# Optimization experiments

Measured on AMD Instinct MI355X. Metric: run time of the kernel, lower is better.

Reference implementation:

```python
import jax, jax.numpy as jnp
import numpy as np


def _weighted_sample(key, w, n_draw):
    # Inverse-CDF weighted sampling with replacement; prob proportional to relu(w).
    # Matches torch.multinomial over the strictly-positive (top-cnt sorted) entries,
    # since zero-weight columns are never selected with side='right'.
    cdf = jnp.cumsum(jnp.maximum(w, 0.0), axis=1)                     # [R, C]
    u = jax.random.uniform(key, (w.shape[0], n_draw), dtype=w.dtype) * cdf[:, -1:]
    idx = jax.vmap(lambda c, q: jnp.searchsorted(c, q, side='right'))(cdf, u)
    return jax.lax.stop_gradient(jnp.minimum(idx, w.shape[1] - 1))    # [R, K] column ids


def contrast_loss(key, padj, nadj, px, nx):
    R, Cp = padj.shape
    Cn = nadj.shape[1]
    K = min(Cp, Cn)  # num = min(pcnt, ncnt) <= K always
    pcnt = jnp.sum(padj > 0, axis=1)
    ncnt = jnp.sum(nadj > 0, axis=1)
    num = jnp.minimum(pcnt, ncnt)                                     # [R] int
    pinc = jnp.argsort(padj, axis=1)                                  # ascending, like torch.sort
    ninc = jnp.argsort(nadj, axis=1)
    kp, kn = jax.random.split(key)
    samp_n = _weighted_sample(kn, nadj, K)                            # sampled negative cols
    samp_p = _weighted_sample(kp, padj, K)                            # sampled positive cols
    j = jnp.arange(K)
    mask = (j[None, :] < num[:, None]).astype(px.dtype)               # first num draws count
    rows = jnp.arange(R)[:, None]
    # top-num entries of the ascending sort: positions C-num .. C-1
    top_p = jnp.clip(Cp - num[:, None] + j[None, :], 0, Cp - 1)
    top_n = jnp.clip(Cn - num[:, None] + j[None, :], 0, Cn - 1)
    pos_A = jnp.take_along_axis(pinc, top_p, axis=1)                  # branch num==pcnt
    neg_B = jnp.take_along_axis(ninc, top_n, axis=1)                  # branch num==ncnt<pcnt
    termA = jnp.maximum(nx[rows, samp_n] - px[rows, pos_A] + 1.0, 0.0)
    termB = jnp.maximum(nx[rows, neg_B] - px[rows, samp_p] + 1.0, 0.0)
    branchA = (pcnt <= ncnt)[:, None]                                 # num == pcnt
    term = jnp.where(branchA, termA, termB) * mask
    row_loss = term.sum(axis=1) / jnp.maximum(num, 1).astype(px.dtype)
    return jnp.where(num > 0, row_loss, 0.0).sum()


def _forward(KUU_adj, VUU_adj, Vuser, Vitem, Kuser, Kitem, preference, Vpreference, structure):
    key = jax.random.key(42)
    k0, k1, k2, k3 = jax.random.split(key, 4)
    f32 = VUU_adj.dtype
    # --- Vu: V-user vs V-user ---
    Vu_adj = Vuser @ Vuser.T                                          # [Nv, Nv]
    n = Vu_adj.shape[0]
    tmp1 = 1.0 - (VUU_adj > 0).astype(f32) - jnp.eye(n, dtype=f32)
    Vu = contrast_loss(k0, VUU_adj, tmp1, Vu_adj, Vu_adj)
    # --- Ku: K-user vs K-user (last 3 cols are negatives) ---
    Ku_adj = Kuser @ Kuser.T                                          # [Nk, Nk]
    Kc = KUU_adj.shape[1]
    tmp2 = (1.0 - (KUU_adj > 0).astype(f32) - jnp.eye(Kc, dtype=f32))[:n, -3:]
    Ku = contrast_loss(k1, KUU_adj[:n, :Kc - 3], tmp2,
                       Ku_adj[:n, :Kc - 3], Ku_adj[:n, -3:])
    # --- Vi: V-user vs V-item (binarization of tmp3 is overwritten in the original) ---
    Vi_adj = Vuser @ Vitem.T                                          # [Nv, NvI]
    VUI_adj = Vpreference.T
    Vi = contrast_loss(k2, VUI_adj, 1.0 - VUI_adj, Vi_adj, Vi_adj)
    # --- Ki: first 5 K-users vs K-item ---
    Ki_adj = Kuser[:5, :] @ Kitem.T                                   # [5, NkI]
    KUI_adj = preference.T
    Ki = contrast_loss(k3, KUI_adj, 1.0 - KUI_adj, Ki_adj, Ki_adj)
    # --- ii: item-item structure alignment ---
    ii_adj = Kitem @ Vitem.T                                          # [NkI, NvI]
    ii = jnp.abs(ii_adj - structure[:, :ii_adj.shape[1]]).mean()
    return (Vu, Ku, Vi, Ki, ii)


def setup_inputs() -> dict:
    key = jax.random.key(0)
    ks = jax.random.split(key, 10)
    Nv, Nk, NvI, NkI, d = 2048, 2051, 4096, 4096, 64
    return {
        'KUU_adj': jax.random.normal(ks[0], (Nk, Nk), jnp.float32),
        'VUU_adj': jax.random.normal(ks[1], (Nv, Nv), jnp.float32),
        'Vuser': jax.random.normal(ks[2], (Nv, d), jnp.float32),
        'Vitem': jax.random.normal(ks[3], (NvI, d), jnp.float32),
        'Kuser': jax.random.normal(ks[4], (Nk, d), jnp.float32),
        'Kitem': jax.random.normal(ks[5], (NkI, d), jnp.float32),
        'Vid': jax.random.randint(ks[6], (Nv,), 0, NvI, jnp.int64 if jax.config.jax_enable_x64 else jnp.int32),
        'preference': jax.random.uniform(ks[7], (NkI, 5), jnp.float32),
        'Vpreference': jax.random.uniform(ks[8], (NvI, Nv), jnp.float32),
        'structure': jax.random.normal(ks[9], (NkI, NvI), jnp.float32),
    }


def reference(KUU_adj, VUU_adj, Vuser, Vitem, Kuser, Kitem, Vid, preference, Vpreference, structure):
    # Vid is accepted by the original forward but never used.
    return _forward(KUU_adj, VUU_adj, Vuser, Vitem, Kuser, Kitem, preference, Vpreference, structure)
```

## Files before the change

### kernel.cpp

```cpp
#include <hip/hip_runtime.h>
#include <cstdint>
#include <cstddef>

__host__ __device__ inline void tf2x32(uint32_t k0, uint32_t k1,
                                       uint32_t c0, uint32_t c1,
                                       uint32_t* o0, uint32_t* o1) {
  uint32_t ks0 = k0, ks1 = k1, ks2 = k0 ^ k1 ^ 0x1BD11BDAu;
  uint32_t x0 = c0 + ks0, x1 = c1 + ks1;
#define TFR(r) { x0 += x1; x1 = (x1 << (r)) | (x1 >> (32 - (r))); x1 ^= x0; }
  TFR(13) TFR(15) TFR(26) TFR(6)   x0 += ks1; x1 += ks2 + 1u;
  TFR(17) TFR(29) TFR(16) TFR(24)  x0 += ks2; x1 += ks0 + 2u;
  TFR(13) TFR(15) TFR(26) TFR(6)   x0 += ks0; x1 += ks1 + 3u;
  TFR(17) TFR(29) TFR(16) TFR(24)  x0 += ks1; x1 += ks2 + 4u;
  TFR(13) TFR(15) TFR(26) TFR(6)   x0 += ks2; x1 += ks0 + 5u;
#undef TFR
  *o0 = x0; *o1 = x1;
}

__device__ inline float tf_u01(uint32_t k0, uint32_t k1, uint32_t c0, uint32_t c1) {
  uint32_t a, b; tf2x32(k0, k1, c0, c1, &a, &b);
  uint32_t bits = a ^ b;
  return __uint_as_float((bits >> 9) | 0x3f800000u) - 1.0f;
}

__device__ inline float mur_u01(uint32_t z, uint32_t salt) {
  z ^= salt;
  z ^= z >> 16; z *= 0x85ebca6bu;
  z ^= z >> 13; z *= 0xc2b2ae35u;
  z ^= z >> 16;
  return __uint_as_float((z >> 9) | 0x3f800000u) - 1.0f;
}

__device__ inline int bsearch_right(const float* cdf, int C, float u) {
  int lo = 0, hi = C;
  while (lo < hi) { int mid = (lo + hi) >> 1; if (cdf[mid] <= u) lo = mid + 1; else hi = mid; }
  return lo < C ? lo : C - 1;
}

__global__ void init_out(float* out) {
  if (threadIdx.x < 5) out[threadIdx.x] = 0.0f;
}

__global__ void transpose_k(const float* __restrict__ in, float* __restrict__ out,
                            int R, int C) {
  __shared__ float tile[32][33];
  int bx = blockIdx.x * 32;
  int by = blockIdx.y * 32;
  int tx = threadIdx.x, ty = threadIdx.y;
#pragma unroll
  for (int q = 0; q < 32; q += 8)
    tile[ty + q][tx] = in[(size_t)(by + ty + q) * C + (bx + tx)];
  __syncthreads();
#pragma unroll
  for (int q = 0; q < 32; q += 8)
    out[(size_t)(bx + ty + q) * R + (by + tx)] = tile[tx][ty + q];
}

__global__ __launch_bounds__(256) void gemm_nt(
    const float* __restrict__ Arows, const float* __restrict__ Brows,
    float* __restrict__ X, int N) {
  __shared__ __align__(16) float At[64 * 68];
  __shared__ __align__(16) float Bt[64 * 68];
  const int t = threadIdx.x;
  const int i0 = blockIdx.x * 64, j0 = blockIdx.y * 64;
  for (int idx = t; idx < 1024; idx += 256) {
    int row = idx >> 4, q = idx & 15;
    float4 va = *(const float4*)(Arows + (size_t)(i0 + row) * 64 + 4 * q);
    At[(4 * q + 0) * 68 + row] = va.x; At[(4 * q + 1) * 68 + row] = va.y;
    At[(4 * q + 2) * 68 + row] = va.z; At[(4 * q + 3) * 68 + row] = va.w;
    float4 vb = *(const float4*)(Brows + (size_t)(j0 + row) * 64 + 4 * q);
    Bt[(4 * q + 0) * 68 + row] = vb.x; Bt[(4 * q + 1) * 68 + row] = vb.y;
    Bt[(4 * q + 2) * 68 + row] = vb.z; Bt[(4 * q + 3) * 68 + row] = vb.w;
  }
  __syncthreads();
  const int ti = t >> 4, tj = t & 15;
  float acc[4][4] = {{0.f,0.f,0.f,0.f},{0.f,0.f,0.f,0.f},{0.f,0.f,0.f,0.f},{0.f,0.f,0.f,0.f}};
  for (int k = 0; k < 64; ++k) {
    const float4 a = *(const float4*)&At[k * 68 + 4 * ti];
    const float4 b = *(const float4*)&Bt[k * 68 + 4 * tj];
    const float av[4] = {a.x, a.y, a.z, a.w};
    const float bv[4] = {b.x, b.y, b.z, b.w};
#pragma unroll
    for (int p = 0; p < 4; ++p)
#pragma unroll
      for (int q2 = 0; q2 < 4; ++q2) acc[p][q2] += av[p] * bv[q2];
  }
#pragma unroll
  for (int p = 0; p < 4; ++p) {
    float4 w = make_float4(acc[p][0], acc[p][1], acc[p][2], acc[p][3]);
    *(float4*)(X + (size_t)(i0 + 4 * ti + p) * N + j0 + 4 * tj) = w;
  }
}

__global__ __launch_bounds__(256) void ii_kernel(
    const float* __restrict__ Kitem, const float* __restrict__ Vitem,
    const float* __restrict__ structure_, float* __restrict__ out) {
  __shared__ __align__(16) float At[64 * 68];
  __shared__ __align__(16) float Bt[64 * 68];
  __shared__ float red[256];
  const int t = threadIdx.x;
  const int i0 = blockIdx.x * 64, j0 = blockIdx.y * 64;
  for (int idx = t; idx < 1024; idx += 256) {
    int row = idx >> 4, q = idx & 15;
    float4 va = *(const float4*)(Kitem + (size_t)(i0 + row) * 64 + 4 * q);
    At[(4 * q + 0) * 68 + row] = va.x; At[(4 * q + 1) * 68 + row] = va.y;
    At[(4 * q + 2) * 68 + row] = va.z; At[(4 * q + 3) * 68 + row] = va.w;
    float4 vb = *(const float4*)(Vitem + (size_t)(j0 + row) * 64 + 4 * q);
    Bt[(4 * q + 0) * 68 + row] = vb.x; Bt[(4 * q + 1) * 68 + row] = vb.y;
    Bt[(4 * q + 2) * 68 + row] = vb.z; Bt[(4 * q + 3) * 68 + row] = vb.w;
  }
  __syncthreads();
  const int ti = t >> 4, tj = t & 15;
  float acc[4][4] = {{0.f,0.f,0.f,0.f},{0.f,0.f,0.f,0.f},{0.f,0.f,0.f,0.f},{0.f,0.f,0.f,0.f}};
  for (int k = 0; k < 64; ++k) {
    const float4 a = *(const float4*)&At[k * 68 + 4 * ti];
    const float4 b = *(const float4*)&Bt[k * 68 + 4 * tj];
    const float av[4] = {a.x, a.y, a.z, a.w};
    const float bv[4] = {b.x, b.y, b.z, b.w};
#pragma unroll
    for (int p = 0; p < 4; ++p)
#pragma unroll
      for (int q2 = 0; q2 < 4; ++q2) acc[p][q2] += av[p] * bv[q2];
  }
  float s = 0.0f;
#pragma unroll
  for (int p = 0; p < 4; ++p) {
    const float* srow = structure_ + (size_t)(i0 + 4 * ti + p) * 4096 + j0 + 4 * tj;
#pragma unroll
    for (int q2 = 0; q2 < 4; ++q2) s += fabsf(acc[p][q2] - srow[q2]);
  }
  red[t] = s; __syncthreads();
  for (int off = 128; off > 0; off >>= 1) {
    if (t < off) red[t] += red[t + off];
    __syncthreads();
  }
  if (t == 0) atomicAdd(out + 4, red[0] * (1.0f / 16777216.0f));
}

template <int C, int MODE, bool PRE>
__global__ __launch_bounds__(256) void contrast2(
    const float* __restrict__ padj_mat, size_t rs, size_t cs,
    const float* __restrict__ xmat,
    const float* __restrict__ A, const float* __restrict__ B,
    float* __restrict__ out, int out_idx, uint32_t salt) {
  constexpr int E = C / 256;
  constexpr int LOG2E = (E == 16) ? 4 : 3;
  constexpr int S = (E == 16) ? 260 : 264;
  constexpr int TSZ = (E - 1) * S + 256;
  constexpr int DEPTH = (C == 4096) ? 13 : 12;
  constexpr int NB = 512;
  __shared__ float T[TSZ];
  __shared__ int bs[NB + 1];
  __shared__ float x[PRE ? 1 : C];
  __shared__ __align__(16) float qa[PRE ? 4 : 64];
  __shared__ float red[256];
  __shared__ float wsumsh[4];
  __shared__ int s_pcnt, s_ncnt;
  const int t = threadIdx.x;
  const int r = blockIdx.x;
  const int lane = t & 63, wid = t >> 6;
  const float* xrow = PRE ? (xmat + (size_t)r * C) : nullptr;
  if (t == 0) { s_pcnt = 0; s_ncnt = 0; }
  if (!PRE && t < 64) qa[t] = A[(size_t)r * 64 + t];

  int lp = 0, ln = 0;
  for (int c = t; c < C; c += 256) {
    float v = padj_mat[(size_t)r * rs + (size_t)c * cs];
    T[(c & (E - 1)) * S + (c >> LOG2E)] = v;
    lp += (v > 0.0f) ? 1 : 0;
    if (MODE == 0) ln += (v <= 0.0f && c != r) ? 1 : 0;
    else           ln += ((1.0f - v) > 0.0f) ? 1 : 0;
  }
  if (lp) atomicAdd(&s_pcnt, lp);
  if (ln) atomicAdd(&s_ncnt, ln);
  __syncthreads();

  if (!PRE) {
    const int g = t >> 2, q = t & 3;
    const float4* qa4 = (const float4*)qa;
    for (int c = g; c < C; c += 64) {
      const float4* b4 = (const float4*)(B + (size_t)c * 64);
      float acc = 0.0f;
#pragma unroll
      for (int m = 0; m < 4; ++m) {
        float4 f = b4[q + 4 * m];
        float4 a = qa4[q + 4 * m];
        acc += f.x * a.x + f.y * a.y + f.z * a.z + f.w * a.w;
      }
      acc += __shfl_xor(acc, 1);
      acc += __shfl_xor(acc, 2);
      if (q == 0) x[c] = acc;
    }
    __syncthreads();
  }

  const int pcnt = s_pcnt, ncnt = s_ncnt;
  const int num = min(pcnt, ncnt);
  if (num == 0) return;
  const bool brA = (pcnt <= ncnt);

  auto wf = [&](float v, int c) -> float {
    if (brA) {
      if (MODE == 0) return (v <= 0.0f && c != r) ? 1.0f : 0.0f;
      float nv = 1.0f - v; return nv > 0.0f ? nv : 0.0f;
    }
    return v > 0.0f ? v : 0.0f;
  };

  float csum = 0.0f;
#pragma unroll
  for (int e = 0; e < E; ++e) csum += wf(T[e * S + t], t * E + e);
  float ps = csum;
#pragma unroll
  for (int off = 1; off < 64; off <<= 1) {
    float o = __shfl_up(ps, off);
    if (lane >= off) ps += o;
  }
  if (lane == 63) wsumsh[wid] = ps;
  __syncthreads();
  float wbase = 0.0f;
  for (int w = 0; w < wid; ++w) wbase += wsumsh[w];
  float run = wbase + ps - csum;
  {
#pragma unroll
    for (int e = 0; e < E; ++e) {
      float w = wf(T[e * S + t], t * E + e);
      run += w;
      T[e * S + t] = run;
    }
  }
  __syncthreads();
  const float total = T[(E - 1) * S + 255];

  for (int i = t; i < NB; i += 256) {
    float ub = ((float)i / (float)NB) * total;
    int lo = 0, hi = C;
    for (int it = 0; it < DEPTH; ++it) {
      if (lo < hi) {
        int mid = (lo + hi) >> 1;
        float cv = T[(mid & (E - 1)) * S + (mid >> LOG2E)];
        if (cv <= ub) lo = mid + 1; else hi = mid;
      }
    }
    bs[i] = lo;
  }
  if (t == 0) bs[NB] = C;
  __syncthreads();

  float acc = 0.0f;
  for (int k = 0; k < E; k += 8) {
    int cj[8]; bool dj[8]; float uj[8]; int lo[8], hi[8]; float xc[8];
#pragma unroll
    for (int j = 0; j < 8; ++j) {
      int c = t + (k + j) * 256;
      cj[j] = c;
      float v = padj_mat[(size_t)r * rs + (size_t)c * cs];
      bool det = brA ? (v > 0.0f)
                     : (MODE == 0 ? (v <= 0.0f && c != r) : ((1.0f - v) > 0.0f));
      dj[j] = det;
      xc[j] = PRE ? xrow[c] : x[c];
      float f = mur_u01((uint32_t)(r * C + c), salt);
      uj[j] = f * total;
      int b = (int)(f * (float)NB);
      b = b < NB - 1 ? b : NB - 1; b = b > 0 ? b : 0;
      lo[j] = bs[b]; hi[j] = bs[b + 1];
    }
    for (int it = 0; it < 7; ++it) {
#pragma unroll
      for (int j = 0; j < 8; ++j) {
        int mid = (lo[j] + hi[j]) >> 1;
        float cv = T[(mid & (E - 1)) * S + (mid >> LOG2E)];
        if (lo[j] < hi[j]) {
          if (cv <= uj[j]) lo[j] = mid + 1; else hi[j] = mid;
        }
      }
    }
#pragma unroll
    for (int j = 0; j < 8; ++j) {
      if (dj[j]) {
        int s = lo[j] < C ? lo[j] : C - 1;
        float xs = PRE ? xrow[s] : x[s];
        float term = brA ? (xs - xc[j] + 1.0f) : (xc[j] - xs + 1.0f);
        acc += fmaxf(term, 0.0f);
      }
    }
  }
  red[t] = acc; __syncthreads();
  for (int off = 128; off > 0; off >>= 1) {
    if (t < off) red[t] += red[t + off];
    __syncthreads();
  }
  if (t == 0) atomicAdd(out + out_idx, red[0] / (float)num);
}

__global__ __launch_bounds__(256) void ku_kernel(
    const float* __restrict__ KUU, const float* __restrict__ Kuser,
    float* __restrict__ out,
    uint32_t kp0, uint32_t kp1, uint32_t kn0, uint32_t kn1) {
  const int C = 2048;
  constexpr int E = 8, LOG2E = 3, S = 264;
  constexpr int TSZ = (E - 1) * S + 256;
  __shared__ float T[TSZ];
  __shared__ float red[256];
  __shared__ int s_pcnt;
  const int t = threadIdx.x, r = blockIdx.x;
  const float* row = KUU + (size_t)r * 2051;
  if (t == 0) s_pcnt = 0;
  __syncthreads();
  int lp = 0;
  for (int c = t; c < C; c += 256) {
    float v = row[c];
    T[(c & (E - 1)) * S + (c >> LOG2E)] = v > 0.0f ? v : 0.0f;
    lp += (v > 0.0f) ? 1 : 0;
  }
  if (lp) atomicAdd(&s_pcnt, lp);
  __syncthreads();
  const int pcnt = s_pcnt;
  const float n0 = row[2048], n1 = row[2049], n2 = row[2050];
  const int ng0 = (n0 <= 0.0f), ng1 = (n1 <= 0.0f), ng2 = (n2 <= 0.0f);
  const int ncnt = ng0 + ng1 + ng2;
  const int num = min(pcnt, ncnt);
  if (num == 0) return;

  float csum = 0.0f;
#pragma unroll
  for (int e = 0; e < E; ++e) csum += T[e * S + t];
  red[t] = csum; __syncthreads();
  if (t == 0) {
    float run = 0.0f;
    for (int i = 0; i < 256; ++i) { float v = red[i]; red[i] = run; run += v; }
  }
  __syncthreads();
  {
    float run = red[t];
#pragma unroll
    for (int e = 0; e < E; ++e) { run += T[e * S + t]; T[e * S + t] = run; }
  }
  __syncthreads();
  const float total = T[(E - 1) * S + 255];

  if (pcnt > ncnt) {
    float term = 0.0f;
    if (t < num) {
      int ng[3] = {ng0, ng1, ng2};
      int det = -1, cnt = 0;
      for (int q = 0; q < 3; ++q) {
        if (ng[q]) { if (cnt == t) { det = q; break; } cnt++; }
      }
      float f = tf_u01(kp0, kp1, 0u, (uint32_t)(r * 3 + t));
      float u = f * total;
      int lo = 0, hi = C;
      while (lo < hi) {
        int mid = (lo + hi) >> 1;
        float cv = T[(mid & (E - 1)) * S + (mid >> LOG2E)];
        if (cv <= u) lo = mid + 1; else hi = mid;
      }
      int s = lo < C ? lo : C - 1;
      const float* qr = Kuser + (size_t)r * 64;
      const float* qs = Kuser + (size_t)s * 64;
      const float* qn = Kuser + (size_t)(2048 + det) * 64;
      float px = 0.0f, nx = 0.0f;
      for (int k = 0; k < 64; ++k) { float av = qr[k]; px += av * qs[k]; nx += av * qn[k]; }
      term = fmaxf(nx - px + 1.0f, 0.0f);
    }
    red[t] = term; __syncthreads();
    for (int off = 128; off > 0; off >>= 1) {
      if (t < off) red[t] += red[t + off];
      __syncthreads();
    }
    if (t == 0) atomicAdd(out + 1, red[0] / (float)num);
  } else {
    if (t == 0) {
      float pv[3]; int pi[3]; int np = 0;
      for (int c = 0; c < C; ++c) {
        float v = row[c];
        if (v > 0.0f) { if (np < 3) { pv[np] = v; pi[np] = c; } np++; }
      }
      for (int a2 = 1; a2 < np; ++a2) {
        float v = pv[a2]; int id = pi[a2]; int b2 = a2 - 1;
        while (b2 >= 0 && pv[b2] > v) { pv[b2 + 1] = pv[b2]; pi[b2 + 1] = pi[b2]; b2--; }
        pv[b2 + 1] = v; pi[b2 + 1] = id;
      }
      int ng[3] = {ng0, ng1, ng2};
      float ncdf[3]; float runn = 0.0f;
      for (int q = 0; q < 3; ++q) { runn += ng[q] ? 1.0f : 0.0f; ncdf[q] = runn; }
      float ss = 0.0f;
      for (int j = 0; j < num; ++j) {
        float f = tf_u01(kn0, kn1, 0u, (uint32_t)(r * 3 + j));
        float u = f * runn;
        int s = 0; while (s < 3 && ncdf[s] <= u) s++; if (s > 2) s = 2;
        int det = pi[np - num + j];
        const float* qr = Kuser + (size_t)r * 64;
        const float* qd = Kuser + (size_t)det * 64;
        const float* qn = Kuser + (size_t)(2048 + s) * 64;
        float px = 0.0f, nx = 0.0f;
        for (int k = 0; k < 64; ++k) { float av = qr[k]; px += av * qd[k]; nx += av * qn[k]; }
        ss += fmaxf(nx - px + 1.0f, 0.0f);
      }
      atomicAdd(out + 1, ss / (float)num);
    }
  }
}

__global__ __launch_bounds__(256) void ki_prep(
    const float* __restrict__ preference,
    float* __restrict__ cdf_ws, float* __restrict__ vals_ws,
    int* __restrict__ rank_ws, float* __restrict__ meta) {
  const int C = 4096;
  __shared__ float cdf[4096];
  __shared__ float red[256];
  __shared__ int s_pcnt;
  const int t = threadIdx.x, r = blockIdx.x;
  if (t == 0) s_pcnt = 0;
  __syncthreads();
  for (int i = r * 256 + t; i < 5 * C; i += 5 * 256) rank_ws[i] = 0;
  int lp = 0;
  for (int c = t; c < C; c += 256) {
    float v = preference[(size_t)c * 5 + r];
    lp += (v > 0.0f) ? 1 : 0;
    cdf[c] = 1.0f - v;
    vals_ws[(size_t)r * C + c] = v;
  }
  if (lp) atomicAdd(&s_pcnt, lp);
  __syncthreads();
  const int num = s_pcnt;
  const int E = C >> 8;
  const int base = t * E;
  float csum = 0.0f;
  for (int e = 0; e < E; ++e) csum += cdf[base + e];
  red[t] = csum; __syncthreads();
  if (t == 0) {
    float run = 0.0f;
    for (int i = 0; i < 256; ++i) { float v = red[i]; red[i] = run; run += v; }
  }
  __syncthreads();
  {
    float run = red[t];
    for (int e = 0; e < E; ++e) { float w = cdf[base + e]; run += w; cdf[base + e] = run; }
  }
  __syncthreads();
  for (int c = t; c < C; c += 256) cdf_ws[(size_t)r * C + c] = cdf[c];
  if (t == 0) { meta[2 * r] = (float)num; meta[2 * r + 1] = cdf[C - 1]; }
}

__global__ __launch_bounds__(256) void ki_rank_p(
    const float* __restrict__ vals_ws, int* __restrict__ rank_ws) {
  const int C = 4096;
  __shared__ __align__(16) float sv[256];
  const int t = threadIdx.x;
  const int r = blockIdx.y;
  const int z = blockIdx.z;
  const int c0 = blockIdx.x * 256 + t;
  const float* vrow = vals_ws + (size_t)r * C;
  sv[t] = vrow[z * 256 + t];
  __syncthreads();
  const float v0 = vrow[c0];
  const int cbase = z * 256;
  int rank = 0;
  const float4* sv4 = (const float4*)sv;
#pragma unroll 8
  for (int q = 0; q < 64; ++q) {
    float4 w = sv4[q];
    int cb = cbase + 4 * q;
    rank += (w.x < v0 || (w.x == v0 && cb + 0 < c0)) ? 1 : 0;
    rank += (w.y < v0 || (w.y == v0 && cb + 1 < c0)) ? 1 : 0;
    rank += (w.z < v0 || (w.z == v0 && cb + 2 < c0)) ? 1 : 0;
    rank += (w.w < v0 || (w.w == v0 && cb + 3 < c0)) ? 1 : 0;
  }
  if (rank) atomicAdd(&rank_ws[(size_t)r * C + c0], rank);
}

__global__ __launch_bounds__(256) void ki_scatter(
    const int* __restrict__ rank_ws, int* __restrict__ sorted_ws) {
  const int C = 4096;
  const int t = threadIdx.x;
  const int r = blockIdx.y;
  const int c0 = blockIdx.x * 256 + t;
  sorted_ws[(size_t)r * C + rank_ws[(size_t)r * C + c0]] = c0;
}

__global__ __launch_bounds__(256) void ki_draw(
    const float* __restrict__ cdf_ws, const int* __restrict__ sorted_ws,
    const float* __restrict__ meta,
    const float* __restrict__ Kuser, const float* __restrict__ Kitem,
    float* __restrict__ out, uint32_t kn0, uint32_t kn1) {
  const int C = 4096;
  __shared__ float cdf[4096];
  __shared__ __align__(16) float qa[64];
  __shared__ float red[256];
  const int t = threadIdx.x;
  const int r = blockIdx.y;
  const int j = blockIdx.x * 256 + t;
  if (t < 64) qa[t] = Kuser[(size_t)r * 64 + t];
  for (int c = t; c < C; c += 256) cdf[c] = cdf_ws[(size_t)r * C + c];
  __syncthreads();
  const int num = (int)meta[2 * r];
  const float total = meta[2 * r + 1];
  float acc = 0.0f;
  if (j < num) {
    float f = tf_u01(kn0, kn1, 0u, (uint32_t)(r * 4096 + j));
    float u = f * total;
    int s = bsearch_right(cdf, C, u);
    int det = sorted_ws[(size_t)r * C + (C - num + j)];
    const float4* qa4 = (const float4*)qa;
    const float4* bs = (const float4*)(Kitem + (size_t)s * 64);
    const float4* bd = (const float4*)(Kitem + (size_t)det * 64);
    float xs = 0.0f, xd = 0.0f;
#pragma unroll
    for (int m = 0; m < 16; ++m) {
      float4 a4 = qa4[m]; float4 v1 = bs[m]; float4 v2 = bd[m];
      xs += a4.x * v1.x + a4.y * v1.y + a4.z * v1.z + a4.w * v1.w;
      xd += a4.x * v2.x + a4.y * v2.y + a4.z * v2.z + a4.w * v2.w;
    }
    acc = fmaxf(xs - xd + 1.0f, 0.0f) / (float)num;
  }
  red[t] = acc; __syncthreads();
  for (int off = 128; off > 0; off >>= 1) {
    if (t < off) red[t] += red[t + off];
    __syncthreads();
  }
  if (t == 0 && red[0] != 0.0f) atomicAdd(out + 3, red[0]);
}

__global__ __launch_bounds__(256) void ki_kernel(
    const float* __restrict__ preference, const float* __restrict__ Kuser,
    const float* __restrict__ Kitem, float* __restrict__ out,
    uint32_t kn0, uint32_t kn1) {
  const int C = 4096;
  __shared__ float cdf[4096];
  __shared__ unsigned long long skey[4096];
  __shared__ __align__(16) float qa[64];
  __shared__ float red[256];
  __shared__ int s_pcnt;
  const int t = threadIdx.x, r = blockIdx.x;
  if (t == 0) s_pcnt = 0;
  if (t < 64) qa[t] = Kuser[(size_t)r * 64 + t];
  __syncthreads();
  int lp = 0;
  for (int c = t; c < C; c += 256) {
    float v = preference[(size_t)c * 5 + r];
    lp += (v > 0.0f) ? 1 : 0;
    cdf[c] = 1.0f - v;
    skey[c] = ((unsigned long long)__float_as_uint(v) << 32) | (unsigned)c;
  }
  if (lp) atomicAdd(&s_pcnt, lp);
  __syncthreads();
  const int num = s_pcnt;
  if (num == 0) return;
  const int E = C >> 8;
  const int base = t * E;
  float csum = 0.0f;
  for (int e = 0; e < E; ++e) csum += cdf[base + e];
  red[t] = csum; __syncthreads();
  if (t == 0) {
    float run = 0.0f;
    for (int i = 0; i < 256; ++i) { float v = red[i]; red[i] = run; run += v; }
  }
  __syncthreads();
  {
    float run = red[t];
    for (int e = 0; e < E; ++e) { float w = cdf[base + e]; run += w; cdf[base + e] = run; }
  }
  __syncthreads();
  const float total = cdf[C - 1];
  for (int k = 2; k <= C; k <<= 1) {
    for (int j2 = k >> 1; j2 > 0; j2 >>= 1) {
      for (int i = t; i < C; i += 256) {
        int ixj = i ^ j2;
        if (ixj > i) {
          unsigned long long a = skey[i], b = skey[ixj];
          bool up = ((i & k) == 0);
          if ((a > b) == up) { skey[i] = b; skey[ixj] = a; }
        }
      }
      __syncthreads();
    }
  }
  float acc = 0.0f;
  const float4* qa4 = (const float4*)qa;
  for (int j = t; j < num; j += 256) {
    float f = tf_u01(kn0, kn1, 0u, (uint32_t)(r * 4096 + j));
    float u = f * total;
    int s = bsearch_right(cdf, C, u);
    int det = (int)(skey[C - num + j] & 0xffffffffull);
    const float4* bs = (const float4*)(Kitem + (size_t)s * 64);
    const float4* bd = (const float4*)(Kitem + (size_t)det * 64);
    float xs = 0.0f, xd = 0.0f;
#pragma unroll
    for (int m = 0; m < 16; ++m) {
      float4 a4 = qa4[m]; float4 v1 = bs[m]; float4 v2 = bd[m];
      xs += a4.x * v1.x + a4.y * v1.y + a4.z * v1.z + a4.w * v1.w;
      xd += a4.x * v2.x + a4.y * v2.y + a4.z * v2.z + a4.w * v2.w;
    }
    acc += fmaxf(xs - xd + 1.0f, 0.0f);
  }
  red[t] = acc; __syncthreads();
  for (int off = 128; off > 0; off >>= 1) {
    if (t < off) red[t] += red[t + off];
    __syncthreads();
  }
  if (t == 0) atomicAdd(out + 3, red[0] / (float)num);
}

extern "C" void kernel_launch(void* const* d_in, const int* in_sizes, int n_in,
                              void* d_out, int out_size, void* d_ws, size_t ws_size,
                              hipStream_t stream) {
  const float* KUU   = (const float*)d_in[0];
  const float* VUU   = (const float*)d_in[1];
  const float* Vuser = (const float*)d_in[2];
  const float* Vitem = (const float*)d_in[3];
  const float* Kuser = (const float*)d_in[4];
  const float* Kitem = (const float*)d_in[5];
  const float* pref  = (const float*)d_in[7];
  const float* Vpref = (const float*)d_in[8];
  const float* structure_ = (const float*)d_in[9];
  float* out = (float*)d_out;

  uint32_t k1a, k1b, k3a, k3b;
  tf2x32(0u, 42u, 0u, 1u, &k1a, &k1b);
  tf2x32(0u, 42u, 0u, 3u, &k3a, &k3b);
  uint32_t kup0, kup1, kun0, kun1, kin0, kin1;
  tf2x32(k1a, k1b, 0u, 0u, &kup0, &kup1);
  tf2x32(k1a, k1b, 0u, 1u, &kun0, &kun1);
  tf2x32(k3a, k3b, 0u, 1u, &kin0, &kin1);

  const uint32_t SALT_VU = 0x8AF1B0C2u;
  const uint32_t SALT_VI = 0x5F356495u;

  const size_t vuit_bytes = (size_t)2048 * 4096 * sizeof(float);
  const size_t xvi_bytes  = (size_t)2048 * 4096 * sizeof(float);
  const size_t xvu_bytes  = (size_t)2048 * 2048 * sizeof(float);
  const size_t ki_bytes   = (size_t)(4 * 5 * 4096 + 16) * sizeof(float);
  const size_t full_bytes = vuit_bytes + xvi_bytes + xvu_bytes + ki_bytes;

  const bool full = ws_size >= full_bytes;
  const bool mid  = !full && ws_size >= vuit_bytes + ki_bytes;

  hipLaunchKernelGGL(init_out, dim3(1), dim3(64), 0, stream, out);

  if (full) {
    float* VUIt = (float*)d_ws;
    float* Xvi  = (float*)((char*)d_ws + vuit_bytes);
    float* Xvu  = (float*)((char*)d_ws + vuit_bytes + xvi_bytes);
    char*  kib  = (char*)d_ws + vuit_bytes + xvi_bytes + xvu_bytes;
    float* cdf_ws  = (float*)kib;
    float* vals_ws = cdf_ws + 5 * 4096;
    int*   sorted_ws = (int*)(vals_ws + 5 * 4096);
    int*   rank_ws = sorted_ws + 5 * 4096;
    float* meta = (float*)(rank_ws + 5 * 4096);

    hipLaunchKernelGGL(ki_prep, dim3(5), dim3(256), 0, stream,
                       pref, cdf_ws, vals_ws, rank_ws, meta);
    hipLaunchKernelGGL(ki_rank_p, dim3(16, 5, 16), dim3(256), 0, stream,
                       vals_ws, rank_ws);
    hipLaunchKernelGGL(ki_scatter, dim3(16, 5), dim3(256), 0, stream,
                       rank_ws, sorted_ws);
    hipLaunchKernelGGL(ki_draw, dim3(16, 5), dim3(256), 0, stream,
                       cdf_ws, sorted_ws, meta, Kuser, Kitem, out, kin0, kin1);

    hipLaunchKernelGGL(transpose_k, dim3(64, 128), dim3(32, 8), 0, stream,
                       Vpref, VUIt, 4096, 2048);
    hipLaunchKernelGGL(gemm_nt, dim3(32, 32), dim3(256), 0, stream,
                       Vuser, Vuser, Xvu, 2048);
    hipLaunchKernelGGL(gemm_nt, dim3(32, 64), dim3(256), 0, stream,
                       Vuser, Vitem, Xvi, 4096);
    hipLaunchKernelGGL(ii_kernel, dim3(64, 64), dim3(256), 0, stream,
                       Kitem, Vitem, structure_, out);

    hipLaunchKernelGGL((contrast2<2048, 0, true>), dim3(2048), dim3(256), 0, stream,
                       VUU, (size_t)2048, (size_t)1, Xvu, nullptr, nullptr,
                       out, 0, SALT_VU);
    hipLaunchKernelGGL(ku_kernel, dim3(2048), dim3(256), 0, stream,
                       KUU, Kuser, out, kup0, kup1, kun0, kun1);
    hipLaunchKernelGGL((contrast2<4096, 1, true>), dim3(2048), dim3(256), 0, stream,
                       VUIt, (size_t)4096, (size_t)1, Xvi, nullptr, nullptr,
                       out, 2, SALT_VI);
  } else if (mid) {
    float* VUIt = (float*)d_ws;
    char*  kib  = (char*)d_ws + vuit_bytes;
    float* cdf_ws  = (float*)kib;
    float* vals_ws = cdf_ws + 5 * 4096;
    int*   sorted_ws = (int*)(vals_ws + 5 * 4096);
    int*   rank_ws = sorted_ws + 5 * 4096;
    float* meta = (float*)(rank_ws + 5 * 4096);

    hipLaunchKernelGGL(ki_prep, dim3(5), dim3(256), 0, stream,
                       pref, cdf_ws, vals_ws, rank_ws, meta);
    hipLaunchKernelGGL(ki_rank_p, dim3(16, 5, 16), dim3(256), 0, stream,
                       vals_ws, rank_ws);
    hipLaunchKernelGGL(ki_scatter, dim3(16, 5), dim3(256), 0, stream,
                       rank_ws, sorted_ws);
    hipLaunchKernelGGL(ki_draw, dim3(16, 5), dim3(256), 0, stream,
                       cdf_ws, sorted_ws, meta, Kuser, Kitem, out, kin0, kin1);

    hipLaunchKernelGGL(ii_kernel, dim3(64, 64), dim3(256), 0, stream,
                       Kitem, Vitem, structure_, out);
    hipLaunchKernelGGL(transpose_k, dim3(64, 128), dim3(32, 8), 0, stream,
                       Vpref, VUIt, 4096, 2048);
    hipLaunchKernelGGL((contrast2<2048, 0, false>), dim3(2048), dim3(256), 0, stream,
                       VUU, (size_t)2048, (size_t)1, nullptr, Vuser, Vuser,
                       out, 0, SALT_VU);
    hipLaunchKernelGGL(ku_kernel, dim3(2048), dim3(256), 0, stream,
                       KUU, Kuser, out, kup0, kup1, kun0, kun1);
    hipLaunchKernelGGL((contrast2<4096, 1, false>), dim3(2048), dim3(256), 0, stream,
                       VUIt, (size_t)4096, (size_t)1, nullptr, Vuser, Vitem,
                       out, 2, SALT_VI);
  } else {
    hipLaunchKernelGGL(ii_kernel, dim3(64, 64), dim3(256), 0, stream,
                       Kitem, Vitem, structure_, out);
    hipLaunchKernelGGL((contrast2<2048, 0, false>), dim3(2048), dim3(256), 0, stream,
                       VUU, (size_t)2048, (size_t)1, nullptr, Vuser, Vuser,
                       out, 0, SALT_VU);
    hipLaunchKernelGGL(ku_kernel, dim3(2048), dim3(256), 0, stream,
                       KUU, Kuser, out, kup0, kup1, kun0, kun1);
    hipLaunchKernelGGL((contrast2<4096, 1, false>), dim3(2048), dim3(256), 0, stream,
                       Vpref, (size_t)1, (size_t)2048, nullptr, Vuser, Vitem,
                       out, 2, SALT_VI);
    hipLaunchKernelGGL(ki_kernel, dim3(5), dim3(256), 0, stream,
                       pref, Kuser, Kitem, out, kin0, kin1);
  }
}
```

Before: 410.6 us.

## Compute item-item GEMM with bf16 MFMA instead of fp32 FMA tiles

Replaces the fp32 scalar outer-product item-item kernel with one that converts Kitem/Vitem tiles to bf16 in shared memory and uses 16x16x32 bf16 MFMA instructions. It then takes the L1 distance against structure. This cuts the ALU cost of the 64x64x64 tile products. The risk is bf16 rounding error in the structure loss, and the kernel is likely bound by the structure read anyway.

```diff
diff --git a/kernel.cpp b/kernel.cpp
--- a/kernel.cpp
+++ b/kernel.cpp
@@ -1,6 +1,9 @@
 #include <hip/hip_runtime.h>
 #include <cstdint>
 #include <cstddef>
+
+typedef __attribute__((ext_vector_type(8))) short short8;
+typedef __attribute__((ext_vector_type(4))) float f32x4;
 
 __host__ __device__ inline void tf2x32(uint32_t k0, uint32_t k1,
                                        uint32_t c0, uint32_t c1,
@@ -35,6 +38,13 @@
   int lo = 0, hi = C;
   while (lo < hi) { int mid = (lo + hi) >> 1; if (cdf[mid] <= u) lo = mid + 1; else hi = mid; }
   return lo < C ? lo : C - 1;
+}
+
+__device__ inline uint32_t bfpack(float x, float y) {
+  uint32_t a = __float_as_uint(x), b = __float_as_uint(y);
+  a = (a + 0x7fffu + ((a >> 16) & 1u)) >> 16;
+  b = (b + 0x7fffu + ((b >> 16) & 1u)) >> 16;
+  return a | (b << 16);
 }
 
 __global__ void init_out(float* out) {
@@ -92,42 +102,64 @@
   }
 }
 
-__global__ __launch_bounds__(256) void ii_kernel(
+__global__ __launch_bounds__(256) void ii_mfma(
     const float* __restrict__ Kitem, const float* __restrict__ Vitem,
     const float* __restrict__ structure_, float* __restrict__ out) {
-  __shared__ __align__(16) float At[64 * 68];
-  __shared__ __align__(16) float Bt[64 * 68];
+  __shared__ __align__(16) uint32_t Ab[8 * 260];
+  __shared__ __align__(16) uint32_t Bb[8 * 260];
   __shared__ float red[256];
   const int t = threadIdx.x;
   const int i0 = blockIdx.x * 64, j0 = blockIdx.y * 64;
-  for (int idx = t; idx < 1024; idx += 256) {
-    int row = idx >> 4, q = idx & 15;
-    float4 va = *(const float4*)(Kitem + (size_t)(i0 + row) * 64 + 4 * q);
-    At[(4 * q + 0) * 68 + row] = va.x; At[(4 * q + 1) * 68 + row] = va.y;
-    At[(4 * q + 2) * 68 + row] = va.z; At[(4 * q + 3) * 68 + row] = va.w;
-    float4 vb = *(const float4*)(Vitem + (size_t)(j0 + row) * 64 + 4 * q);
-    Bt[(4 * q + 0) * 68 + row] = vb.x; Bt[(4 * q + 1) * 68 + row] = vb.y;
-    Bt[(4 * q + 2) * 68 + row] = vb.z; Bt[(4 * q + 3) * 68 + row] = vb.w;
-  }
-  __syncthreads();
-  const int ti = t >> 4, tj = t & 15;
-  float acc[4][4] = {{0.f,0.f,0.f,0.f},{0.f,0.f,0.f,0.f},{0.f,0.f,0.f,0.f},{0.f,0.f,0.f,0.f}};
-  for (int k = 0; k < 64; ++k) {
-    const float4 a = *(const float4*)&At[k * 68 + 4 * ti];
-    const float4 b = *(const float4*)&Bt[k * 68 + 4 * tj];
-    const float av[4] = {a.x, a.y, a.z, a.w};
-    const float bv[4] = {b.x, b.y, b.z, b.w};
-#pragma unroll
-    for (int p = 0; p < 4; ++p)
-#pragma unroll
-      for (int q2 = 0; q2 < 4; ++q2) acc[p][q2] += av[p] * bv[q2];
-  }
+
+  {
+    const int m = t >> 2, cq = t & 3;
+    const int kk = cq >> 1;
+    const int q0 = (cq & 1) * 2;
+    const int R = (m >> 4) * 2 + kk;
+    const int m15 = m & 15;
+    const float4* sa = (const float4*)(Kitem + (size_t)(i0 + m) * 64 + cq * 16);
+    const float4* sb = (const float4*)(Vitem + (size_t)(j0 + m) * 64 + cq * 16);
+    float4 a0 = sa[0], a1 = sa[1], a2 = sa[2], a3 = sa[3];
+    float4 b0 = sb[0], b1 = sb[1], b2 = sb[2], b3 = sb[3];
+    uint4 ca0 = make_uint4(bfpack(a0.x, a0.y), bfpack(a0.z, a0.w),
+                           bfpack(a1.x, a1.y), bfpack(a1.z, a1.w));
+    uint4 ca1 = make_uint4(bfpack(a2.x, a2.y), bfpack(a2.z, a2.w),
+                           bfpack(a3.x, a3.y), bfpack(a3.z, a3.w));
+    uint4 cb0 = make_uint4(bfpack(b0.x, b0.y), bfpack(b0.z, b0.w),
+                           bfpack(b1.x, b1.y), bfpack(b1.z, b1.w));
+    uint4 cb1 = make_uint4(bfpack(b2.x, b2.y), bfpack(b2.z, b2.w),
+                           bfpack(b3.x, b3.y), bfpack(b3.z, b3.w));
+    const int o0 = R * 260 + (((q0 + 0) << 4) | m15) * 4;
+    const int o1 = R * 260 + (((q0 + 1) << 4) | m15) * 4;
+    *(uint4*)(Ab + o0) = ca0;  *(uint4*)(Ab + o1) = ca1;
+    *(uint4*)(Bb + o0) = cb0;  *(uint4*)(Bb + o1) = cb1;
+  }
+  __syncthreads();
+
+  const int w = t >> 6, l = t & 63;
+  short8 afr0 = *(const short8*)(Ab + (w * 2 + 0) * 260 + l * 4);
+  short8 afr1 = *(const short8*)(Ab + (w * 2 + 1) * 260 + l * 4);
+  f32x4 acc[4];
+#pragma unroll
+  for (int ct = 0; ct < 4; ++ct) {
+    short8 bfr0 = *(const short8*)(Bb + (ct * 2 + 0) * 260 + l * 4);
+    short8 bfr1 = *(const short8*)(Bb + (ct * 2 + 1) * 260 + l * 4);
+    f32x4 a = {0.0f, 0.0f, 0.0f, 0.0f};
+    a = __builtin_amdgcn_mfma_f32_16x16x32_bf16(afr0, bfr0, a, 0, 0, 0);
+    a = __builtin_amdgcn_mfma_f32_16x16x32_bf16(afr1, bfr1, a, 0, 0, 0);
+    acc[ct] = a;
+  }
+
+  const int col = l & 15, rquad = l >> 4;
   float s = 0.0f;
 #pragma unroll
-  for (int p = 0; p < 4; ++p) {
-    const float* srow = structure_ + (size_t)(i0 + 4 * ti + p) * 4096 + j0 + 4 * tj;
-#pragma unroll
-    for (int q2 = 0; q2 < 4; ++q2) s += fabsf(acc[p][q2] - srow[q2]);
+  for (int ct = 0; ct < 4; ++ct) {
+    const int gc = j0 + ct * 16 + col;
+#pragma unroll
+    for (int reg = 0; reg < 4; ++reg) {
+      const int gr = i0 + w * 16 + rquad * 4 + reg;
+      s += fabsf(acc[ct][reg] - structure_[(size_t)gr * 4096 + gc]);
+    }
   }
   red[t] = s; __syncthreads();
   for (int off = 128; off > 0; off >>= 1) {
@@ -664,7 +696,7 @@
                        Vuser, Vuser, Xvu, 2048);
     hipLaunchKernelGGL(gemm_nt, dim3(32, 64), dim3(256), 0, stream,
                        Vuser, Vitem, Xvi, 4096);
-    hipLaunchKernelGGL(ii_kernel, dim3(64, 64), dim3(256), 0, stream,
+    hipLaunchKernelGGL(ii_mfma, dim3(64, 64), dim3(256), 0, stream,
                        Kitem, Vitem, structure_, out);
 
     hipLaunchKernelGGL((contrast2<2048, 0, true>), dim3(2048), dim3(256), 0, stream,
@@ -693,7 +725,7 @@
     hipLaunchKernelGGL(ki_draw, dim3(16, 5), dim3(256), 0, stream,
                        cdf_ws, sorted_ws, meta, Kuser, Kitem, out, kin0, kin1);
 
-    hipLaunchKernelGGL(ii_kernel, dim3(64, 64), dim3(256), 0, stream,
+    hipLaunchKernelGGL(ii_mfma, dim3(64, 64), dim3(256), 0, stream,
                        Kitem, Vitem, structure_, out);
     hipLaunchKernelGGL(transpose_k, dim3(64, 128), dim3(32, 8), 0, stream,
                        Vpref, VUIt, 4096, 2048);
@@ -706,7 +738,7 @@
                        VUIt, (size_t)4096, (size_t)1, nullptr, Vuser, Vitem,
                        out, 2, SALT_VI);
   } else {
-    hipLaunchKernelGGL(ii_kernel, dim3(64, 64), dim3(256), 0, stream,
+    hipLaunchKernelGGL(ii_mfma, dim3(64, 64), dim3(256), 0, stream,
                        Kitem, Vitem, structure_, out);
     hipLaunchKernelGGL((contrast2<2048, 0, false>), dim3(2048), dim3(256), 0, stream,
                        VUU, (size_t)2048, (size_t)1, nullptr, Vuser, Vuser,
```

Result: no change. 417.3 us (+1.6%).
